# Kernel tuning notes

Hardware: AMD Instinct MI355X
Metric: run time of the kernel (lower is better)

Reference implementation:

```python
import jax, jax.numpy as jnp
import numpy as np

B, S = 512, 64          # batch, grain grid size (coarse==medium==fine==64, see notes)
N = S * S               # tokens per image
CONTENT_PAD, CONTENT_EOS = 1024, 1025
COARSE_POS_PAD, COARSE_POS_EOS = 128, 129
MEDIUM_POS_PAD, MEDIUM_POS_EOS = 256, 257
FINE_POS_PAD, FINE_POS_EOS = 1024, 1025


def setup_inputs() -> dict:
    key = jax.random.key(0)
    k1, k2 = jax.random.split(key)
    indices = jax.random.randint(k1, (B, S, S), 0, 1024, dtype=jnp.int32)
    grain_indices = jax.random.randint(k2, (B, S, S), 0, 3, dtype=jnp.int32)
    return {"indices": indices, "grain_indices": grain_indices}


def _compact(vals, mask, eos, pad):
    """Stable stream-compaction per row: selected vals first, then EOS, then PAD.
    vals/mask: [B, N].  Output: [B, N+1] (static max length; torch pads to batch max)."""
    b, n = vals.shape
    # stable argsort of (not mask) brings True positions to the front, in order
    order = jnp.argsort(jnp.where(mask, 0, 1).astype(jnp.int32), axis=1, stable=True)
    sel = jnp.take_along_axis(vals, order, axis=1)                  # [B, N]
    sel = jnp.concatenate([sel, jnp.zeros((b, 1), vals.dtype)], axis=1)  # [B, N+1]
    cnt = jnp.sum(mask.astype(jnp.int32), axis=1, keepdims=True)    # [B, 1]
    slot = jnp.arange(n + 1, dtype=jnp.int32)[None, :]              # [1, N+1]
    out = jnp.where(slot < cnt, sel,
                    jnp.where(slot == cnt, jnp.asarray(eos, vals.dtype),
                              jnp.asarray(pad, vals.dtype)))
    return out


def reference(indices, grain_indices):
    b, s, _ = indices.shape
    n = s * s
    # With coarse==medium==fine the module's rearranges are identity reshapes:
    # coarse_content = medium_content source = fine_content source = flattened grid,
    # and all three position sequences are row-major arange(n).
    flat = indices.reshape(b, n)
    g = grain_indices.reshape(b, n)
    pos = jnp.broadcast_to(jnp.arange(n, dtype=indices.dtype), (b, n))

    coarse_content = _compact(flat, g == 0, CONTENT_EOS, CONTENT_PAD)
    coarse_position = _compact(pos, g == 0, COARSE_POS_EOS, COARSE_POS_PAD)
    medium_content = _compact(flat, g == 1, CONTENT_EOS, CONTENT_PAD)
    medium_position = _compact(pos, g == 1, MEDIUM_POS_EOS, MEDIUM_POS_PAD)
    fine_content = _compact(flat, g == 2, CONTENT_EOS, CONTENT_PAD)
    fine_position = _compact(pos, g == 2, FINE_POS_EOS, FINE_POS_PAD)

    coarse_segment = jnp.zeros_like(coarse_content)
    medium_segment = jnp.ones_like(medium_content)
    fine_segment = jnp.full_like(fine_content, 2)
    return (coarse_content, medium_content, fine_content,
            coarse_position, medium_position, fine_position,
            coarse_segment, medium_segment, fine_segment)
```

## Files before the change

### kernel.cpp

```cpp
#include <hip/hip_runtime.h>


constexpr int N_TOK  = 4096;
constexpr int M_OUT  = N_TOK + 1;
constexpr int TPB    = 256;
constexpr int EPT    = N_TOK / TPB;

constexpr int CONTENT_PAD = 1024, CONTENT_EOS = 1025;
__device__ __constant__ int POS_PAD[3] = {128, 256, 1024};
__device__ __constant__ int POS_EOS[3] = {129, 257, 1025};

__global__ __launch_bounds__(TPB) void
triple_grain_permute(const int* __restrict__ indices,
                     const int* __restrict__ grain,
                     int* __restrict__ out,
                     int batch) {
    const int b = blockIdx.x;
    const int t = threadIdx.x;
    const int lane = t & 63;
    const int wave = t >> 6;

    const int* idx_row = indices + (size_t)b * N_TOK;
    const int* g_row   = grain   + (size_t)b * N_TOK;

    __shared__ int s_content[N_TOK];
    __shared__ int s_pos[N_TOK];
    __shared__ unsigned long long s_wave_tot[4];

    int gv[EPT], iv[EPT];
    {
        const int4* g4 = reinterpret_cast<const int4*>(g_row + t * EPT);
        const int4* i4 = reinterpret_cast<const int4*>(idx_row + t * EPT);
#pragma unroll
        for (int k = 0; k < EPT / 4; ++k) {
            int4 gg = g4[k];
            int4 ii = i4[k];
            gv[4 * k + 0] = gg.x; gv[4 * k + 1] = gg.y;
            gv[4 * k + 2] = gg.z; gv[4 * k + 3] = gg.w;
            iv[4 * k + 0] = ii.x; iv[4 * k + 1] = ii.y;
            iv[4 * k + 2] = ii.z; iv[4 * k + 3] = ii.w;
        }
    }

    int c0 = 0, c1 = 0, c2 = 0;
#pragma unroll
    for (int j = 0; j < EPT; ++j) {
        c0 += (gv[j] == 0);
        c1 += (gv[j] == 1);
        c2 += (gv[j] == 2);
    }
    unsigned long long packed =
        (unsigned long long)c0 |
        ((unsigned long long)c1 << 21) |
        ((unsigned long long)c2 << 42);

    unsigned long long inc = packed;
#pragma unroll
    for (int off = 1; off < 64; off <<= 1) {
        unsigned long long nb =
            (unsigned long long)__shfl_up((long long)inc, off, 64);
        if (lane >= off) inc += nb;
    }
    if (lane == 63) s_wave_tot[wave] = inc;
    __syncthreads();

    unsigned long long wave_prefix = 0, total = 0;
#pragma unroll
    for (int w = 0; w < 4; ++w) {
        unsigned long long v = s_wave_tot[w];
        if (w < wave) wave_prefix += v;
        total += v;
    }
    const unsigned long long excl = wave_prefix + (inc - packed);

    const int o0 = (int)(excl & 0x1FFFFF);
    const int o1 = (int)((excl >> 21) & 0x1FFFFF);
    const int o2 = (int)((excl >> 42) & 0x1FFFFF);
    const int cnt0 = (int)(total & 0x1FFFFF);
    const int cnt1 = (int)((total >> 21) & 0x1FFFFF);
    const int cnt2 = (int)((total >> 42) & 0x1FFFFF);

    const int base0 = 0, base1 = cnt0, base2 = cnt0 + cnt1;

    int d0 = base0 + o0, d1 = base1 + o1, d2 = base2 + o2;
    const int elem0 = t * EPT;
#pragma unroll
    for (int j = 0; j < EPT; ++j) {
        const int c = gv[j];
        const int dst = (c == 0) ? d0 : ((c == 1) ? d1 : d2);
        s_content[dst] = iv[j];
        s_pos[dst]     = elem0 + j;
        d0 += (c == 0);
        d1 += (c == 1);
        d2 += (c == 2);
    }
    __syncthreads();

    const size_t ARR = (size_t)batch * M_OUT;
    const int bases[3] = {base0, base1, base2};
    const int cnts[3]  = {cnt0, cnt1, cnt2};

#pragma unroll
    for (int c = 0; c < 3; ++c) {
        int* dst_c = out + (size_t)c       * ARR + (size_t)b * M_OUT;
        int* dst_p = out + (size_t)(3 + c) * ARR + (size_t)b * M_OUT;
        int* dst_s = out + (size_t)(6 + c) * ARR + (size_t)b * M_OUT;
        const int cnt = cnts[c];
        const int base = bases[c];
        const int peos = POS_EOS[c], ppad = POS_PAD[c];
        for (int slot = t; slot < M_OUT; slot += TPB) {
            int vc, vp;
            if (slot < cnt) {
                vc = s_content[base + slot];
                vp = s_pos[base + slot];
            } else if (slot == cnt) {
                vc = CONTENT_EOS;
                vp = peos;
            } else {
                vc = CONTENT_PAD;
                vp = ppad;
            }
            dst_c[slot] = vc;
            dst_p[slot] = vp;
            dst_s[slot] = c;
        }
    }
}

extern "C" void kernel_launch(void* const* d_in, const int* in_sizes, int n_in,
                              void* d_out, int out_size, void* d_ws, size_t ws_size,
                              hipStream_t stream) {
    const int* indices = (const int*)d_in[0];
    const int* grain   = (const int*)d_in[1];
    int* out = (int*)d_out;

    const int batch = in_sizes[0] / N_TOK;
    triple_grain_permute<<<batch, TPB, 0, stream>>>(indices, grain, out, batch);
}
```

Measured before the change: 92.92 us.

## Use 1024-thread blocks and pack content and position into one LDS word

Raises block size from 256 to 1024 threads so each thread handles 4 tokens with a single int4 load per input, and widens the cross-wave scan to 16 waves. Content (under 4096) and position are packed into one 32-bit word in shared memory, halving LDS footprint and LDS traffic during scatter and gather. This aims to increase parallelism and occupancy for a kernel bound by writing the output. The packing relies on content values fitting in 12 bits, and the larger block makes the wave-total reduction loop longer.

```diff
diff --git a/kernel.cpp b/kernel.cpp
--- a/kernel.cpp
+++ b/kernel.cpp
@@ -3,14 +3,15 @@
 
 constexpr int N_TOK  = 4096;
 constexpr int M_OUT  = N_TOK + 1;
-constexpr int TPB    = 256;
+constexpr int TPB    = 1024;
+constexpr int NWAVES = TPB / 64;
 constexpr int EPT    = N_TOK / TPB;
 
 constexpr int CONTENT_PAD = 1024, CONTENT_EOS = 1025;
 __device__ __constant__ int POS_PAD[3] = {128, 256, 1024};
 __device__ __constant__ int POS_EOS[3] = {129, 257, 1025};
 
-__global__ __launch_bounds__(TPB) void
+__global__ __launch_bounds__(TPB, 8) void
 triple_grain_permute(const int* __restrict__ indices,
                      const int* __restrict__ grain,
                      int* __restrict__ out,
@@ -23,24 +24,17 @@
     const int* idx_row = indices + (size_t)b * N_TOK;
     const int* g_row   = grain   + (size_t)b * N_TOK;
 
-    __shared__ int s_content[N_TOK];
-    __shared__ int s_pos[N_TOK];
-    __shared__ unsigned long long s_wave_tot[4];
+    __shared__ int s_packed[N_TOK];
+    __shared__ unsigned long long s_wave_tot[NWAVES];
 
-    int gv[EPT], iv[EPT];
-    {
-        const int4* g4 = reinterpret_cast<const int4*>(g_row + t * EPT);
-        const int4* i4 = reinterpret_cast<const int4*>(idx_row + t * EPT);
-#pragma unroll
-        for (int k = 0; k < EPT / 4; ++k) {
-            int4 gg = g4[k];
-            int4 ii = i4[k];
-            gv[4 * k + 0] = gg.x; gv[4 * k + 1] = gg.y;
-            gv[4 * k + 2] = gg.z; gv[4 * k + 3] = gg.w;
-            iv[4 * k + 0] = ii.x; iv[4 * k + 1] = ii.y;
-            iv[4 * k + 2] = ii.z; iv[4 * k + 3] = ii.w;
-        }
-    }
+    int4 gg = reinterpret_cast<const int4*>(g_row)[t];
+    int4 ii = reinterpret_cast<const int4*>(idx_row)[t];
+    int gv[EPT] = {gg.x, gg.y, gg.z, gg.w};
+    const int elem0 = t * EPT;
+    int pv[EPT] = {ii.x | (elem0 << 12),
+                   ii.y | ((elem0 + 1) << 12),
+                   ii.z | ((elem0 + 2) << 12),
+                   ii.w | ((elem0 + 3) << 12)};
 
     int c0 = 0, c1 = 0, c2 = 0;
 #pragma unroll
@@ -66,7 +60,7 @@
 
     unsigned long long wave_prefix = 0, total = 0;
 #pragma unroll
-    for (int w = 0; w < 4; ++w) {
+    for (int w = 0; w < NWAVES; ++w) {
         unsigned long long v = s_wave_tot[w];
         if (w < wave) wave_prefix += v;
         total += v;
@@ -83,13 +77,11 @@
     const int base0 = 0, base1 = cnt0, base2 = cnt0 + cnt1;
 
     int d0 = base0 + o0, d1 = base1 + o1, d2 = base2 + o2;
-    const int elem0 = t * EPT;
 #pragma unroll
     for (int j = 0; j < EPT; ++j) {
         const int c = gv[j];
         const int dst = (c == 0) ? d0 : ((c == 1) ? d1 : d2);
-        s_content[dst] = iv[j];
-        s_pos[dst]     = elem0 + j;
+        s_packed[dst] = pv[j];
         d0 += (c == 0);
         d1 += (c == 1);
         d2 += (c == 2);
@@ -111,8 +103,9 @@
         for (int slot = t; slot < M_OUT; slot += TPB) {
             int vc, vp;
             if (slot < cnt) {
-                vc = s_content[base + slot];
-                vp = s_pos[base + slot];
+                const int p = s_packed[base + slot];
+                vc = p & 0xFFF;
+                vp = p >> 12;
             } else if (slot == cnt) {
                 vc = CONTENT_EOS;
                 vp = peos;
```

Result: faster. 91.00 us (-2.1%).
